# Performance work log

Measured on AMD Instinct MI355X. Metric: run time of the kernel, lower is better.

The kernel has to match this reference:

```python
import jax, jax.numpy as jnp
import numpy as np

S, B, D, H = 512, 16, 512, 8  # seq_len, batch, d_model, n_heads
DH = D // H


def setup_inputs() -> dict:
    key = jax.random.key(0)
    k1, k2, k3, k4, k5 = jax.random.split(key, 5)
    x = jax.random.normal(k1, (S, B, D), dtype=jnp.float32)
    # nn.MultiheadAttention params: packed in_proj [3D, D], out_proj [D, D]
    W_in = jax.random.normal(k2, (3 * D, D), dtype=jnp.float32) * (D ** -0.5)
    b_in = jax.random.normal(k3, (3 * D,), dtype=jnp.float32) * 0.02
    W_out = jax.random.normal(k4, (D, D), dtype=jnp.float32) * (D ** -0.5)
    b_out = jax.random.normal(k5, (D,), dtype=jnp.float32) * 0.02
    return {"x": x, "W_in": W_in, "b_in": b_in, "W_out": W_out, "b_out": b_out}


def _mha(q_in, k_in, v_in, W_in, b_in, W_out, b_out):
    """torch.nn.MultiheadAttention (batch_first=False, eval mode). Inputs: (S, B, D)."""
    Wq, Wk, Wv = jnp.split(W_in, 3, axis=0)
    bq, bk, bv = jnp.split(b_in, 3)

    def heads(t):  # (S, B, D) -> (B, H, S, DH)
        s, b, _ = t.shape
        return t.reshape(s, b, H, DH).transpose(1, 2, 0, 3)

    q = heads(q_in @ Wq.T + bq) * (DH ** -0.5)
    k = heads(k_in @ Wk.T + bk)
    v = heads(v_in @ Wv.T + bv)
    attn = jax.nn.softmax(jnp.einsum('bhsd,bhtd->bhst', q, k), axis=-1)
    o = jnp.einsum('bhst,bhtd->bhsd', attn, v)          # (B, H, S, DH)
    o = o.transpose(2, 0, 1, 3).reshape(q_in.shape)      # (S, B, D)
    return o @ W_out.T + b_out


def reference(x, W_in, b_in, W_out, b_out):
    ch = jnp.arange(x.shape[-1])  # channel indices of last dim

    def step(acc, i):
        # x_i: only channel i kept (mirrors x_i[..., i] = x[..., i])
        x_i = jnp.where(ch == i, x, 0.0)
        # x_i_prime = where(x_i == 0, x, 0): x with channel i zeroed (where nonzero)
        x_ip = jnp.where(x_i == 0.0, x, 0.0)
        out = _mha(x_i, x_ip, x_ip, W_in, b_in, W_out, b_out)
        return acc + out, None

    # loop runs x.size(1) times, exactly as the torch code
    acc, _ = jax.lax.scan(step, jnp.zeros_like(x), jnp.arange(x.shape[1]))
    return acc
```

## Files before the change

kernel.cpp:

```cpp
#include <hip/hip_runtime.h>

#define S_LEN 512
#define BATCH 16
#define DMODEL 512
#define NHEAD 8
#define DH 64
#define NI 16

typedef float f32x4 __attribute__((ext_vector_type(4)));
typedef float f32x2 __attribute__((ext_vector_type(2)));
typedef short s16x8 __attribute__((ext_vector_type(8)));

__device__ __forceinline__ unsigned short f2bf(float f){
  unsigned int u = __float_as_uint(f);
  u += 0x7FFFu + ((u >> 16) & 1u);
  return (unsigned short)(u >> 16);
}

__device__ __forceinline__ void async16(const unsigned short* g, unsigned short* l){
  __builtin_amdgcn_global_load_lds(
      (const __attribute__((address_space(1))) unsigned int*)g,
      (__attribute__((address_space(3))) unsigned int*)l, 16, 0, 0);
}

template<int CTRL>
__device__ __forceinline__ float dppAdd(float x){
  int v = __builtin_amdgcn_update_dpp(0, __float_as_int(x), CTRL, 0xF, 0xF, true);
  return x + __int_as_float(v);
}

__device__ __forceinline__ void plswap32(float &a, float &b){
  asm("v_permlane32_swap_b32 %0, %1" : "+v"(a), "+v"(b));
}
__device__ __forceinline__ void plswap16(float &a, float &b){
  asm("v_permlane16_swap_b32 %0, %1" : "+v"(a), "+v"(b));
}
__device__ __forceinline__ unsigned int cvtpk_bf16(float lo, float hi){
  unsigned int r;
  asm("v_cvt_pk_bf16_f32 %0, %1, %2" : "=v"(r) : "v"(lo), "v"(hi));
  return r;
}
__device__ __forceinline__ f32x2 pk_fma(f32x2 a, f32x2 b, f32x2 c){
  f32x2 d;
  asm("v_pk_fma_f32 %0, %1, %2, %3" : "=v"(d) : "v"(a), "v"(b), "v"(c));
  return d;
}
__device__ __forceinline__ f32x2 pk_add(f32x2 a, f32x2 b){
  f32x2 d;
  asm("v_pk_add_f32 %0, %1, %2" : "=v"(d) : "v"(a), "v"(b));
  return d;
}

__global__ void k_prep(const float* __restrict__ x, unsigned short* __restrict__ xb,
                       float* __restrict__ zcol, const float* __restrict__ Win,
                       const float* __restrict__ Wout, unsigned short* __restrict__ Winb,
                       unsigned short* __restrict__ Wob){
  int bidx = blockIdx.x;
  if (bidx < 4096){
    int tid = bidx * 256 + threadIdx.x;
    float4 v = reinterpret_cast<const float4*>(x)[tid];
    ushort4 o;
    o.x = f2bf(v.x); o.y = f2bf(v.y); o.z = f2bf(v.z); o.w = f2bf(v.w);
    reinterpret_cast<ushort4*>(xb)[tid] = o;
    int d0 = (tid & 127) * 4;
    if (d0 < 16){
      int row = tid >> 7;
      int t = row >> 4, b = row & 15;
      zcol[(size_t)(b * 16 + d0 + 0) * 512 + t] = v.x;
      zcol[(size_t)(b * 16 + d0 + 1) * 512 + t] = v.y;
      zcol[(size_t)(b * 16 + d0 + 2) * 512 + t] = v.z;
      zcol[(size_t)(b * 16 + d0 + 3) * 512 + t] = v.w;
    }
  } else if (bidx < 4864){
    int t = (bidx - 4096) * 256 + threadIdx.x;
    float4 v = reinterpret_cast<const float4*>(Win)[t];
    ushort4 o;
    o.x = f2bf(v.x); o.y = f2bf(v.y); o.z = f2bf(v.z); o.w = f2bf(v.w);
    reinterpret_cast<ushort4*>(Winb)[t] = o;
  } else {
    int t = (bidx - 4864) * 256 + threadIdx.x;
    float4 v = reinterpret_cast<const float4*>(Wout)[t];
    ushort4 o;
    o.x = f2bf(v.x); o.y = f2bf(v.y); o.z = f2bf(v.z); o.w = f2bf(v.w);
    reinterpret_cast<ushort4*>(Wob)[t] = o;
  }
}

__global__ __launch_bounds__(256) void k_kv2(const unsigned short* __restrict__ xb,
    const unsigned short* __restrict__ Winb, const float* __restrict__ b_in,
    float* __restrict__ Kf, unsigned short* __restrict__ Vfb){
  __shared__ unsigned short As[2][128 * 32];
  __shared__ unsigned short Bs[2][128 * 32];
  int tid = threadIdx.x;
  int w = tid >> 6, l = tid & 63;
  int ln = l & 15, kb = l >> 4;
  int wr = w >> 1, wc = w & 1;
  int m0 = blockIdx.x * 128;
  int n0 = blockIdx.y * 128;
  const unsigned short* Brow = Winb + (size_t)512 * DMODEL;

  f32x4 acc[4][4];
  #pragma unroll
  for (int mi = 0; mi < 4; ++mi)
    #pragma unroll
    for (int nj = 0; nj < 4; ++nj) acc[mi][nj] = (f32x4){0.f,0.f,0.f,0.f};

  int c0 = tid, c1 = 256 + tid;
  int r0 = c0 >> 2, q0 = c0 & 3, r1 = c1 >> 2, q1 = c1 & 3;
  int lb0 = (w * 64) * 8, lb1 = (256 + w * 64) * 8;

  #define STAGE_KV(kt, buf) do { int k0 = (kt) * 32;                                   \
    async16(xb   + (size_t)(m0 + r0) * DMODEL + k0 + q0 * 8, &As[buf][lb0]);           \
    async16(xb   + (size_t)(m0 + r1) * DMODEL + k0 + q1 * 8, &As[buf][lb1]);           \
    async16(Brow + (size_t)(n0 + r0) * DMODEL + k0 + q0 * 8, &Bs[buf][lb0]);           \
    async16(Brow + (size_t)(n0 + r1) * DMODEL + k0 + q1 * 8, &Bs[buf][lb1]);           \
  } while(0)

  STAGE_KV(0, 0);
  __syncthreads();
  int cur = 0;
  for (int kt = 0; kt < 16; ++kt){
    if (kt < 15) STAGE_KV(kt + 1, cur ^ 1);
    const unsigned short* Ab = &As[cur][(wr * 64 + ln) * 32 + kb * 8];
    const unsigned short* Bb = &Bs[cur][(wc * 64 + ln) * 32 + kb * 8];
    s16x8 af[4], bf[4];
    #pragma unroll
    for (int mi = 0; mi < 4; ++mi) af[mi] = *reinterpret_cast<const s16x8*>(Ab + mi * 16 * 32);
    #pragma unroll
    for (int nj = 0; nj < 4; ++nj) bf[nj] = *reinterpret_cast<const s16x8*>(Bb + nj * 16 * 32);
    #pragma unroll
    for (int mi = 0; mi < 4; ++mi)
      #pragma unroll
      for (int nj = 0; nj < 4; ++nj)
        acc[mi][nj] = __builtin_amdgcn_mfma_f32_16x16x32_bf16(af[mi], bf[nj], acc[mi][nj], 0, 0, 0);
    __syncthreads();
    cur ^= 1;
  }
  #undef STAGE_KV

  #pragma unroll
  for (int nj = 0; nj < 4; ++nj){
    int n = n0 + wc * 64 + nj * 16 + ln;
    float bias = b_in[512 + n];
    #pragma unroll
    for (int mi = 0; mi < 4; ++mi){
      #pragma unroll
      for (int r = 0; r < 4; ++r){
        int m = m0 + wr * 64 + mi * 16 + kb * 4 + r;
        float v = acc[mi][nj][r] + bias;
        if (n < DMODEL) Kf[(size_t)m * DMODEL + n] = v;
        else            Vfb[(size_t)m * DMODEL + (n - DMODEL)] = f2bf(v);
      }
    }
  }
}

__global__ void k_tr(const unsigned short* __restrict__ Vfb, unsigned short* __restrict__ VfT){
  __shared__ unsigned short tile[32][34];
  int b = blockIdx.z; int t0 = blockIdx.x * 32; int d0 = blockIdx.y * 32;
  int tx = threadIdx.x & 31, ty = threadIdx.x >> 5;
  #pragma unroll
  for (int k = 0; k < 4; ++k){
    int row = ty + 8 * k;
    tile[row][tx] = Vfb[(size_t)((t0 + row) * BATCH + b) * DMODEL + d0 + tx];
  }
  __syncthreads();
  #pragma unroll
  for (int k = 0; k < 4; ++k){
    int row = ty + 8 * k;
    VfT[(size_t)b * (DMODEL * S_LEN) + (size_t)(d0 + row) * S_LEN + t0 + tx] = tile[tx][row];
  }
}

__global__ __launch_bounds__(256) void k_gh(const float* __restrict__ W_in,
    const float* __restrict__ b_in, const float* __restrict__ Kf,
    const float* __restrict__ zcol, float* __restrict__ G, float* __restrict__ H){
  const float SCALE = 0.18033688011112042f;
  int bh = blockIdx.x >> 1, th = blockIdx.x & 1;
  int b = bh >> 3, h = bh & 7;
  __shared__ float u[64][17];
  __shared__ float cvec[64];
  __shared__ float alpha[16], beta[16];
  int tid = threadIdx.x;
  for (int idx = tid; idx < 1024; idx += 256){
    int d = idx >> 4, i = idx & 15;
    u[d][i] = W_in[(size_t)(h * 64 + d) * DMODEL + i];
  }
  if (tid < 64) cvec[tid] = b_in[h * 64 + tid];
  __syncthreads();
  if (tid < 16){
    float a = 0.f, be = 0.f;
    for (int d = 0; d < 64; ++d){
      float wk = W_in[(size_t)(512 + h * 64 + d) * DMODEL + tid];
      a  += u[d][tid] * wk;
      be += cvec[d] * wk;
    }
    alpha[tid] = a; beta[tid] = be;
  }
  __syncthreads();
  int t = th * 256 + tid;
  float K[64];
  const float* kp = Kf + (size_t)(t * BATCH + b) * DMODEL + h * 64;
  #pragma unroll
  for (int d = 0; d < 64; d += 4){
    float4 v = *reinterpret_cast<const float4*>(kp + d);
    K[d] = v.x; K[d+1] = v.y; K[d+2] = v.z; K[d+3] = v.w;
  }
  float Bt = 0.f;
  #pragma unroll
  for (int d = 0; d < 64; ++d) Bt += cvec[d] * K[d];
  for (int i = 0; i < 16; ++i){
    float A = 0.f;
    #pragma unroll
    for (int d = 0; d < 64; ++d) A += u[d][i] * K[d];
    float z = zcol[(size_t)(b * 16 + i) * 512 + t];
    G[(size_t)(bh * 16 + i) * 512 + t] = (A  - alpha[i] * z) * SCALE;
    H[(size_t)(bh * 16 + i) * 512 + t] = (Bt - beta[i]  * z) * SCALE;
  }
}

__global__ __launch_bounds__(512) void k_smpv(const float* __restrict__ G,
    const float* __restrict__ H, const float* __restrict__ zcol,
    const unsigned short* __restrict__ VfT, const float* __restrict__ W_in,
    unsigned short* __restrict__ Ob){
  __shared__ unsigned short Pl[32 * 512];
  __shared__ float Rs[32][17];
  __shared__ float Wvl[64][17];
  int j = blockIdx.x;
  int xcd = j & 7, rest = j >> 3;
  int bh_hi = rest & 15, sb = rest >> 4;
  int bh = bh_hi * 8 + xcd;
  int b = bh >> 3, h = bh & 7;
  int tid = threadIdx.x, w = tid >> 6, l = tid & 63;

  for (int idx = tid; idx < 1024; idx += 512){
    int d = idx >> 4, i = idx & 15;
    Wvl[d][i] = W_in[(size_t)(2 * DMODEL + h * 64 + d) * DMODEL + i];
  }

  const float* gb = G    + ((size_t)bh * NI) * S_LEN;
  const float* hb = H    + ((size_t)bh * NI) * S_LEN;
  const float* zb = zcol + ((size_t)b  * NI) * S_LEN;
  int t0 = l * 4, t1 = 256 + l * 4;
  int s_w = sb * 32 + w * 4;

  f32x2 Pacc[4][4];
  #pragma unroll
  for (int r = 0; r < 4; ++r)
    #pragma unroll
    for (int jp = 0; jp < 4; ++jp) Pacc[r][jp] = (f32x2){0.f, 0.f};

  for (int i = 0; i < NI; ++i){
    const float* gp = gb + (i << 9);
    const float* hp = hb + (i << 9);
    const float* zp = zb + (i << 9);
    f32x4 gA = *reinterpret_cast<const f32x4*>(gp + t0);
    f32x4 gB = *reinterpret_cast<const f32x4*>(gp + t1);
    f32x4 hA = *reinterpret_cast<const f32x4*>(hp + t0);
    f32x4 hB = *reinterpret_cast<const f32x4*>(hp + t1);
    f32x4 zA = *reinterpret_cast<const f32x4*>(zp + t0);
    f32x4 zB = *reinterpret_cast<const f32x4*>(zp + t1);
    float4 y4 = *reinterpret_cast<const float4*>(zp + s_w);
    f32x2 g2[4] = {gA.lo, gA.hi, gB.lo, gB.hi};
    f32x2 h2[4] = {hA.lo, hA.hi, hB.lo, hB.hi};
    f32x2 z2[4] = {zA.lo, zA.hi, zB.lo, zB.hi};
    float ys[4] = {y4.x, y4.y, y4.z, y4.w};

    f32x2 E[4][4];
    float pd[4], pr[4];
    #pragma unroll
    for (int r = 0; r < 4; ++r){
      f32x2 yv = {ys[r], ys[r]};
      f32x2 dacc = {0.f, 0.f}, racc = {0.f, 0.f};
      #pragma unroll
      for (int jp = 0; jp < 4; ++jp){
        f32x2 a = pk_fma(yv, g2[jp], h2[jp]);
        f32x2 e;
        e.x = __builtin_amdgcn_exp2f(a.x);
        e.y = __builtin_amdgcn_exp2f(a.y);
        E[r][jp] = e;
        dacc = pk_add(dacc, e);
        racc = pk_fma(e, z2[jp], racc);
      }
      pd[r] = dacc.x + dacc.y;
      pr[r] = racc.x + racc.y;
    }

    plswap32(pd[0], pd[2]);  float dq0 = pd[0] + pd[2];
    plswap32(pd[1], pd[3]);  float dq1 = pd[1] + pd[3];
    plswap32(pr[0], pr[2]);  float rq0 = pr[0] + pr[2];
    plswap32(pr[1], pr[3]);  float rq1 = pr[1] + pr[3];
    plswap16(dq0, dq1);      float du = dq0 + dq1;
    plswap16(rq0, rq1);      float ru = rq0 + rq1;
    du = dppAdd<0x140>(du); ru = dppAdd<0x140>(ru);
    du = dppAdd<0x141>(du); ru = dppAdd<0x141>(ru);
    du = dppAdd<0x4E>(du);  ru = dppAdd<0x4E>(ru);
    du = dppAdd<0xB1>(du);  ru = dppAdd<0xB1>(ru);
    float inv = __builtin_amdgcn_rcpf(du);
    if ((l & 15) == 0)
      Rs[w * 4 + (l >> 4)][i] = ru * inv;
    #pragma unroll
    for (int r = 0; r < 4; ++r){
      float ir = __int_as_float(__builtin_amdgcn_readlane(__float_as_int(inv), 16 * r));
      f32x2 iv = {ir, ir};
      #pragma unroll
      for (int jp = 0; jp < 4; ++jp) Pacc[r][jp] = pk_fma(E[r][jp], iv, Pacc[r][jp]);
    }
  }

  #pragma unroll
  for (int r = 0; r < 4; ++r){
    int sl = w * 4 + r;
    unsigned int u0 = cvtpk_bf16(Pacc[r][0].x, Pacc[r][0].y);
    unsigned int u1 = cvtpk_bf16(Pacc[r][1].x, Pacc[r][1].y);
    unsigned int u2 = cvtpk_bf16(Pacc[r][2].x, Pacc[r][2].y);
    unsigned int u3 = cvtpk_bf16(Pacc[r][3].x, Pacc[r][3].y);
    int xr = (sl & 7) << 4;
    char* rowp = (char*)Pl + sl * 1024;
    uint2 v01; v01.x = u0; v01.y = u1;
    uint2 v23; v23.x = u2; v23.y = u3;
    *reinterpret_cast<uint2*>(rowp + ((l * 8) ^ xr)) = v01;
    *reinterpret_cast<uint2*>(rowp + ((512 + l * 8) ^ xr)) = v23;
  }
  __syncthreads();

  int ln = l & 15, kb = l >> 4;
  int sh = (w & 1) * 16;
  int dt = (w >> 1) * 16;
  const unsigned short* bp = VfT + (size_t)b * (DMODEL * S_LEN)
                             + (size_t)(h * 64 + dt + ln) * S_LEN + kb * 8;
  char* arow = (char*)Pl + (sh + ln) * 1024;
  int xa = (ln & 7) << 4;
  f32x4 acc = {0.f, 0.f, 0.f, 0.f};
  #pragma unroll
  for (int kt = 0; kt < 16; ++kt){
    s16x8 af = *reinterpret_cast<const s16x8*>(arow + ((kt * 64 + kb * 16) ^ xa));
    s16x8 bf = *reinterpret_cast<const s16x8*>(bp + kt * 32);
    acc = __builtin_amdgcn_mfma_f32_16x16x32_bf16(af, bf, acc, 0, 0, 0);
  }
  #pragma unroll
  for (int r = 0; r < 4; ++r){
    int sl = sh + kb * 4 + r;
    float corr = 0.f;
    #pragma unroll
    for (int i = 0; i < 16; ++i) corr += Rs[sl][i] * Wvl[dt + ln][i];
    float v = acc[r] - corr;
    int m = sb * 32 + sl;
    Ob[(size_t)(m * BATCH + b) * DMODEL + h * 64 + dt + ln] = f2bf(v);
  }
}

__global__ __launch_bounds__(256) void k_out2(const unsigned short* __restrict__ Ob,
    const unsigned short* __restrict__ Wob, const float* __restrict__ b_out,
    float* __restrict__ out){
  __shared__ unsigned short As[2][128 * 32];
  __shared__ unsigned short Bs[2][128 * 32];
  int tid = threadIdx.x;
  int w = tid >> 6, l = tid & 63;
  int ln = l & 15, kb = l >> 4;
  int wr = w >> 1, wc = w & 1;
  int m0 = blockIdx.x * 128;
  int n0 = blockIdx.y * 128;

  f32x4 acc[4][4];
  #pragma unroll
  for (int mi = 0; mi < 4; ++mi)
    #pragma unroll
    for (int nj = 0; nj < 4; ++nj) acc[mi][nj] = (f32x4){0.f,0.f,0.f,0.f};

  int c0 = tid, c1 = 256 + tid;
  int r0 = c0 >> 2, q0 = c0 & 3, r1 = c1 >> 2, q1 = c1 & 3;
  int lb0 = (w * 64) * 8, lb1 = (256 + w * 64) * 8;

  #define STAGE_O(kt, buf) do { int k0 = (kt) * 32;                                    \
    async16(Ob  + (size_t)(m0 + r0) * DMODEL + k0 + q0 * 8, &As[buf][lb0]);            \
    async16(Ob  + (size_t)(m0 + r1) * DMODEL + k0 + q1 * 8, &As[buf][lb1]);            \
    async16(Wob + (size_t)(n0 + r0) * DMODEL + k0 + q0 * 8, &Bs[buf][lb0]);            \
    async16(Wob + (size_t)(n0 + r1) * DMODEL + k0 + q1 * 8, &Bs[buf][lb1]);            \
  } while(0)

  STAGE_O(0, 0);
  __syncthreads();
  int cur = 0;
  for (int kt = 0; kt < 16; ++kt){
    if (kt < 15) STAGE_O(kt + 1, cur ^ 1);
    const unsigned short* Ab = &As[cur][(wr * 64 + ln) * 32 + kb * 8];
    const unsigned short* Bb = &Bs[cur][(wc * 64 + ln) * 32 + kb * 8];
    s16x8 af[4], bf[4];
    #pragma unroll
    for (int mi = 0; mi < 4; ++mi) af[mi] = *reinterpret_cast<const s16x8*>(Ab + mi * 16 * 32);
    #pragma unroll
    for (int nj = 0; nj < 4; ++nj) bf[nj] = *reinterpret_cast<const s16x8*>(Bb + nj * 16 * 32);
    #pragma unroll
    for (int mi = 0; mi < 4; ++mi)
      #pragma unroll
      for (int nj = 0; nj < 4; ++nj)
        acc[mi][nj] = __builtin_amdgcn_mfma_f32_16x16x32_bf16(af[mi], bf[nj], acc[mi][nj], 0, 0, 0);
    __syncthreads();
    cur ^= 1;
  }
  #undef STAGE_O

  #pragma unroll
  for (int nj = 0; nj < 4; ++nj){
    int n = n0 + wc * 64 + nj * 16 + ln;
    float bias = 16.0f * b_out[n];
    #pragma unroll
    for (int mi = 0; mi < 4; ++mi){
      #pragma unroll
      for (int r = 0; r < 4; ++r){
        int m = m0 + wr * 64 + mi * 16 + kb * 4 + r;
        out[(size_t)m * DMODEL + n] = acc[mi][nj][r] + bias;
      }
    }
  }
}

extern "C" void kernel_launch(void* const* d_in, const int* in_sizes, int n_in,
                              void* d_out, int out_size, void* d_ws, size_t ws_size,
                              hipStream_t stream) {
  const float* x     = (const float*)d_in[0];
  const float* W_in  = (const float*)d_in[1];
  const float* b_in  = (const float*)d_in[2];
  const float* W_out = (const float*)d_in[3];
  const float* b_out = (const float*)d_in[4];
  float* out = (float*)d_out;

  size_t off = 0;
  char* base = (char*)d_ws;
  auto alloc = [&](size_t bytes) -> void* {
    void* p = base + off;
    off += (bytes + 255) & ~(size_t)255;
    return p;
  };
  unsigned short* xb   = (unsigned short*)alloc(8388608);
  unsigned short* Winb = (unsigned short*)alloc(1572864);
  unsigned short* Wob  = (unsigned short*)alloc(524288);
  float*          zcol = (float*)alloc(524288);
  float*          Kf   = (float*)alloc(16777216);
  unsigned short* Vfb  = (unsigned short*)alloc(8388608);
  unsigned short* VfT  = (unsigned short*)alloc(8388608);
  float*          G    = (float*)alloc(4194304);
  float*          H    = (float*)alloc(4194304);
  unsigned short* Ob   = (unsigned short*)alloc(8388608);

  k_prep<<<5120, 256, 0, stream>>>(x, xb, zcol, W_in, W_out, Winb, Wob);

  { dim3 g(64, 8); k_kv2<<<g, 256, 0, stream>>>(xb, Winb, b_in, Kf, Vfb); }
  { dim3 g(16, 16, 16); k_tr<<<g, 256, 0, stream>>>(Vfb, VfT); }
  k_gh<<<256, 256, 0, stream>>>(W_in, b_in, Kf, zcol, G, H);

  k_smpv<<<2048, 512, 0, stream>>>(G, H, zcol, VfT, W_in, Ob);

  { dim3 g(64, 4); k_out2<<<g, 256, 0, stream>>>(Ob, Wob, b_out, out); }
}
```

Measured before the change: 183.1 us.

## Run per-channel PV MFMA inside the softmax loop with double-buffered P tiles

```diff
diff --git a/kernel.cpp b/kernel.cpp
--- a/kernel.cpp
+++ b/kernel.cpp
@@ -39,16 +39,6 @@
   unsigned int r;
   asm("v_cvt_pk_bf16_f32 %0, %1, %2" : "=v"(r) : "v"(lo), "v"(hi));
   return r;
-}
-__device__ __forceinline__ f32x2 pk_fma(f32x2 a, f32x2 b, f32x2 c){
-  f32x2 d;
-  asm("v_pk_fma_f32 %0, %1, %2, %3" : "=v"(d) : "v"(a), "v"(b), "v"(c));
-  return d;
-}
-__device__ __forceinline__ f32x2 pk_add(f32x2 a, f32x2 b){
-  f32x2 d;
-  asm("v_pk_add_f32 %0, %1, %2" : "=v"(d) : "v"(a), "v"(b));
-  return d;
 }
 
 __global__ void k_prep(const float* __restrict__ x, unsigned short* __restrict__ xb,
@@ -223,7 +213,7 @@
     const float* __restrict__ H, const float* __restrict__ zcol,
     const unsigned short* __restrict__ VfT, const float* __restrict__ W_in,
     unsigned short* __restrict__ Ob){
-  __shared__ unsigned short Pl[32 * 512];
+  __shared__ unsigned short Pl[2][32 * 512];
   __shared__ float Rs[32][17];
   __shared__ float Wvl[64][17];
   int j = blockIdx.x;
@@ -244,11 +234,17 @@
   int t0 = l * 4, t1 = 256 + l * 4;
   int s_w = sb * 32 + w * 4;
 
-  f32x2 Pacc[4][4];
-  #pragma unroll
-  for (int r = 0; r < 4; ++r)
-    #pragma unroll
-    for (int jp = 0; jp < 4; ++jp) Pacc[r][jp] = (f32x2){0.f, 0.f};
+  int ln = l & 15, kb = l >> 4;
+  int sh = (w & 1) * 16;
+  int dt = (w >> 1) * 16;
+  int xa = (ln & 7) << 4;
+  const unsigned short* bp = VfT + (size_t)b * (DMODEL * S_LEN)
+                             + (size_t)(h * 64 + dt + ln) * S_LEN + kb * 8;
+  s16x8 Bf[16];
+  #pragma unroll
+  for (int kt = 0; kt < 16; ++kt) Bf[kt] = *reinterpret_cast<const s16x8*>(bp + kt * 32);
+
+  f32x4 oacc = {0.f, 0.f, 0.f, 0.f};
 
   for (int i = 0; i < NI; ++i){
     const float* gp = gb + (i << 9);
@@ -266,7 +262,6 @@
     f32x2 z2[4] = {zA.lo, zA.hi, zB.lo, zB.hi};
     float ys[4] = {y4.x, y4.y, y4.z, y4.w};
 
-    f32x2 E[4][4];
     float pd[4], pr[4];
     #pragma unroll
     for (int r = 0; r < 4; ++r){
@@ -274,13 +269,12 @@
       f32x2 dacc = {0.f, 0.f}, racc = {0.f, 0.f};
       #pragma unroll
       for (int jp = 0; jp < 4; ++jp){
-        f32x2 a = pk_fma(yv, g2[jp], h2[jp]);
+        f32x2 a = yv * g2[jp] + h2[jp];
         f32x2 e;
         e.x = __builtin_amdgcn_exp2f(a.x);
         e.y = __builtin_amdgcn_exp2f(a.y);
-        E[r][jp] = e;
-        dacc = pk_add(dacc, e);
-        racc = pk_fma(e, z2[jp], racc);
+        dacc += e;
+        racc += e * z2[jp];
       }
       pd[r] = dacc.x + dacc.y;
       pr[r] = racc.x + racc.y;
@@ -299,52 +293,50 @@
     float inv = __builtin_amdgcn_rcpf(du);
     if ((l & 15) == 0)
       Rs[w * 4 + (l >> 4)][i] = ru * inv;
+
+    char* bufbase = (char*)&Pl[i & 1][0];
     #pragma unroll
     for (int r = 0; r < 4; ++r){
       float ir = __int_as_float(__builtin_amdgcn_readlane(__float_as_int(inv), 16 * r));
       f32x2 iv = {ir, ir};
-      #pragma unroll
-      for (int jp = 0; jp < 4; ++jp) Pacc[r][jp] = pk_fma(E[r][jp], iv, Pacc[r][jp]);
-    }
-  }
-
-  #pragma unroll
-  for (int r = 0; r < 4; ++r){
-    int sl = w * 4 + r;
-    unsigned int u0 = cvtpk_bf16(Pacc[r][0].x, Pacc[r][0].y);
-    unsigned int u1 = cvtpk_bf16(Pacc[r][1].x, Pacc[r][1].y);
-    unsigned int u2 = cvtpk_bf16(Pacc[r][2].x, Pacc[r][2].y);
-    unsigned int u3 = cvtpk_bf16(Pacc[r][3].x, Pacc[r][3].y);
-    int xr = (sl & 7) << 4;
-    char* rowp = (char*)Pl + sl * 1024;
-    uint2 v01; v01.x = u0; v01.y = u1;
-    uint2 v23; v23.x = u2; v23.y = u3;
-    *reinterpret_cast<uint2*>(rowp + ((l * 8) ^ xr)) = v01;
-    *reinterpret_cast<uint2*>(rowp + ((512 + l * 8) ^ xr)) = v23;
-  }
-  __syncthreads();
-
-  int ln = l & 15, kb = l >> 4;
-  int sh = (w & 1) * 16;
-  int dt = (w >> 1) * 16;
-  const unsigned short* bp = VfT + (size_t)b * (DMODEL * S_LEN)
-                             + (size_t)(h * 64 + dt + ln) * S_LEN + kb * 8;
-  char* arow = (char*)Pl + (sh + ln) * 1024;
-  int xa = (ln & 7) << 4;
-  f32x4 acc = {0.f, 0.f, 0.f, 0.f};
-  #pragma unroll
-  for (int kt = 0; kt < 16; ++kt){
-    s16x8 af = *reinterpret_cast<const s16x8*>(arow + ((kt * 64 + kb * 16) ^ xa));
-    s16x8 bf = *reinterpret_cast<const s16x8*>(bp + kt * 32);
-    acc = __builtin_amdgcn_mfma_f32_16x16x32_bf16(af, bf, acc, 0, 0, 0);
-  }
+      f32x2 yv = {ys[r], ys[r]};
+      f32x2 a0 = yv * g2[0] + h2[0];
+      f32x2 a1 = yv * g2[1] + h2[1];
+      f32x2 a2 = yv * g2[2] + h2[2];
+      f32x2 a3 = yv * g2[3] + h2[3];
+      f32x2 e0 = {__builtin_amdgcn_exp2f(a0.x), __builtin_amdgcn_exp2f(a0.y)}; e0 *= iv;
+      f32x2 e1 = {__builtin_amdgcn_exp2f(a1.x), __builtin_amdgcn_exp2f(a1.y)}; e1 *= iv;
+      f32x2 e2 = {__builtin_amdgcn_exp2f(a2.x), __builtin_amdgcn_exp2f(a2.y)}; e2 *= iv;
+      f32x2 e3 = {__builtin_amdgcn_exp2f(a3.x), __builtin_amdgcn_exp2f(a3.y)}; e3 *= iv;
+      unsigned int u0 = cvtpk_bf16(e0.x, e0.y);
+      unsigned int u1 = cvtpk_bf16(e1.x, e1.y);
+      unsigned int u2 = cvtpk_bf16(e2.x, e2.y);
+      unsigned int u3 = cvtpk_bf16(e3.x, e3.y);
+      int sl = w * 4 + r;
+      int xr = (sl & 7) << 4;
+      char* rowp = bufbase + sl * 1024;
+      uint2 v01; v01.x = u0; v01.y = u1;
+      uint2 v23; v23.x = u2; v23.y = u3;
+      *reinterpret_cast<uint2*>(rowp + ((l * 8) ^ xr)) = v01;
+      *reinterpret_cast<uint2*>(rowp + ((512 + l * 8) ^ xr)) = v23;
+    }
+    __syncthreads();
+
+    char* arow = bufbase + (sh + ln) * 1024;
+    #pragma unroll
+    for (int kt = 0; kt < 16; ++kt){
+      s16x8 af = *reinterpret_cast<const s16x8*>(arow + ((kt * 64 + kb * 16) ^ xa));
+      oacc = __builtin_amdgcn_mfma_f32_16x16x32_bf16(af, Bf[kt], oacc, 0, 0, 0);
+    }
+  }
+
   #pragma unroll
   for (int r = 0; r < 4; ++r){
     int sl = sh + kb * 4 + r;
     float corr = 0.f;
     #pragma unroll
     for (int i = 0; i < 16; ++i) corr += Rs[sl][i] * Wvl[dt + ln][i];
-    float v = acc[r] - corr;
+    float v = oacc[r] - corr;
     int m = sb * 32 + sl;
     Ob[(size_t)(m * BATCH + b) * DMODEL + h * 64 + dt + ln] = f2bf(v);
   }
```

Result: slower. 305.6 us (+66.9%).
